# Performance work log

Hardware: AMD Instinct MI355X
Metric: run time of the kernel (lower is better)

## Reference

```python
import jax, jax.numpy as jnp
import numpy as np

NTOKEN, NINP, NHID = 50257, 256, 256
B, T = 64, 2048
RES, FC1 = 10, NHID // 3
EPS = 1e-5

def lrelu(x, p=0.01):
    return jnp.maximum(x, x * p)

def setup_inputs() -> dict:
    key = jax.random.key(0)
    ks = jax.random.split(key, 12)
    s = 0.05
    inp = {
        "input": jax.random.randint(ks[0], (B, T), 0, NTOKEN),
        "hx": jnp.zeros((B, NHID), jnp.float32),
        "cx": jnp.zeros((B, NHID), jnp.float32),
        "seq_len": jax.random.randint(ks[1], (B,), 1, T + 1),  # lengths in [1, T]
        "emb_w": jax.random.uniform(ks[2], (NTOKEN, NINP), jnp.float32, -0.1, 0.1),
        "W_ih": jax.random.normal(ks[3], (4 * NHID, NINP), jnp.float32) * s,
        "W_hh": jax.random.normal(ks[4], (4 * NHID, NHID), jnp.float32) * s,
        "b_ih": jnp.zeros((4 * NHID,), jnp.float32),
        "b_hh": jnp.zeros((4 * NHID,), jnp.float32),
        "rfc1_w": jax.random.normal(ks[5], (RES, NHID), jnp.float32) * s,
        "rfc1_b": jnp.zeros((RES,), jnp.float32),
        "rbn_g": jnp.ones((RES,), jnp.float32),
        "rbn_b": jnp.zeros((RES,), jnp.float32),
        "rbn_rm": jnp.zeros((RES,), jnp.float32),
        "rbn_rv": jnp.ones((RES,), jnp.float32),
        "rfc2_w": jax.random.normal(ks[6], (NHID, RES), jnp.float32) * s,
        "rfc2_b": jnp.zeros((NHID,), jnp.float32),
        "fc1_w": jax.random.normal(ks[7], (FC1, NHID), jnp.float32) * s,
        "fc1_b": jnp.zeros((FC1,), jnp.float32),
        "bn1_g": jnp.ones((FC1,), jnp.float32),
        "bn1_b": jnp.zeros((FC1,), jnp.float32),
        "bn1_rm": jnp.zeros((FC1,), jnp.float32),
        "bn1_rv": jnp.ones((FC1,), jnp.float32),
        "fc2_w": jax.random.normal(ks[8], (2, FC1), jnp.float32) * s,
        "fc2_b": jnp.zeros((2,), jnp.float32),
    }
    return inp

def reference(input, hx, cx, seq_len, emb_w, W_ih, W_hh, b_ih, b_hh,
              rfc1_w, rfc1_b, rbn_g, rbn_b, rbn_rm, rbn_rv, rfc2_w, rfc2_b,
              fc1_w, fc1_b, bn1_g, bn1_b, bn1_rm, bn1_rv, fc2_w, fc2_b):
    # eval mode: dropout = identity, noise = 0, BatchNorm uses running stats
    emb = emb_w[input.T]  # [T, B, ninp]
    # precompute input-side gates once (batched matmul) -> [T, B, 4*nhid]
    x_gates = jnp.einsum('tbi,gi->tbg', emb, W_ih) + b_ih + b_hh

    def step(carry, xg):
        h, c = carry
        gates = xg + h @ W_hh.T
        i, f, g, o = jnp.split(gates, 4, axis=-1)
        c = jax.nn.sigmoid(f) * c + jax.nn.sigmoid(i) * jnp.tanh(g)
        h = jax.nn.sigmoid(o) * jnp.tanh(c)
        return (h, c), h

    (hx_f, cx_f), outs = jax.lax.scan(step, (hx, cx), x_gates)  # outs: [T, B, nhid]

    # ragged mean pooling over first seq_len[b] steps
    mask = (jnp.arange(T)[:, None] < seq_len[None, :]).astype(outs.dtype)  # [T, B]
    feature = jnp.einsum('tbh,tb->bh', outs, mask) / seq_len[:, None].astype(outs.dtype)

    # ResNet block (eval)
    res = jax.nn.relu(feature) @ rfc1_w.T + rfc1_b
    res = jax.nn.relu(res)
    res = (res - rbn_rm) * jax.lax.rsqrt(rbn_rv + EPS) * rbn_g + rbn_b
    feature = feature + res @ rfc2_w.T + rfc2_b

    # classifier head
    fc = feature @ fc1_w.T + fc1_b
    fc = (fc - bn1_rm) * jax.lax.rsqrt(bn1_rv + EPS) * bn1_g + bn1_b
    fc = lrelu(fc)
    logits = fc @ fc2_w.T + fc2_b
    logp = jax.nn.log_softmax(logits, axis=-1)
    return (logp, hx_f, cx_f)
```

## Files before the change

### kernel.cpp

```cpp
#include <hip/hip_runtime.h>
#include <cstdint>


#define NTOKEN 50257
#define NINP 256
#define NHID 256
#define BB 64
#define TT 2048
#define NRES 10
#define NFC1 85
#define EPSV 1e-5f

typedef _Float16 f16;
typedef _Float16 f16x2 __attribute__((ext_vector_type(2)));
typedef _Float16 f16x8 __attribute__((ext_vector_type(8)));
typedef float f32x4 __attribute__((ext_vector_type(4)));

static __device__ __forceinline__ float sigm(float x) { return 1.0f / (1.0f + __expf(-x)); }
static __device__ __forceinline__ float tanh_(float x) {
  float ax = fabsf(x);
  float e = __expf(-2.0f * ax);
  float t = (1.0f - e) / (1.0f + e);
  return x < 0.0f ? -t : t;
}

static __device__ __forceinline__ float fdot2(f16x2 a, f16x2 b, float c) {
#if __has_builtin(__builtin_amdgcn_fdot2)
  return __builtin_amdgcn_fdot2(a, b, c, false);
#else
  return c + (float)a[0] * (float)b[0] + (float)a[1] * (float)b[1];
#endif
}

__global__ void k0_convert(const float* __restrict__ emb_w, const float* __restrict__ W_ih,
                           const float* __restrict__ b_ih, const float* __restrict__ b_hh,
                           f16* __restrict__ emb16, f16* __restrict__ wih16,
                           float* __restrict__ bias) {
  int64_t i = (int64_t)blockIdx.x * blockDim.x + threadIdx.x;
  if (i < (int64_t)NTOKEN * NINP) emb16[i] = (f16)emb_w[i];
  if (i < 4 * NHID * NINP) wih16[i] = (f16)W_ih[i];
  if (i < 4 * NHID) bias[i] = b_ih[i] + b_hh[i];
}

__global__ __launch_bounds__(256) void k1_gemm(const f16* __restrict__ emb16,
                                               const f16* __restrict__ wih16,
                                               const float* __restrict__ bias,
                                               f16* __restrict__ xgtab) {
  __shared__ __align__(16) f16 a_lds[64][40];
  __shared__ __align__(16) f16 b_lds[256][40];
  const int mt = blockIdx.x;
  const int nt0 = blockIdx.y * 256;
  const int tid = threadIdx.x;
  const int lane = tid & 63;
  const int w = tid >> 6;
  const int quad = lane >> 4;
  const int l16 = lane & 15;

  f32x4 acc[16];
#pragma unroll
  for (int i = 0; i < 16; i++) acc[i] = (f32x4){0.f, 0.f, 0.f, 0.f};

  const int ar = tid >> 2;
  int av = mt * 64 + ar;
  if (av > NTOKEN - 1) av = NTOKEN - 1;
  const int ac = (tid & 3) * 8;

  for (int kb = 0; kb < 256; kb += 32) {
    *(uint4*)&a_lds[ar][ac] = *(const uint4*)&emb16[av * 256 + kb + ac];
    {
      const uint4* bs = (const uint4*)&wih16[(nt0 + tid) * 256 + kb];
      uint4* bd = (uint4*)&b_lds[tid][0];
      bd[0] = bs[0]; bd[1] = bs[1]; bd[2] = bs[2]; bd[3] = bs[3];
    }
    __syncthreads();
    f16x8 af = *(const f16x8*)&a_lds[w * 16 + l16][quad * 8];
#pragma unroll
    for (int nt = 0; nt < 16; nt++) {
      f16x8 bf = *(const f16x8*)&b_lds[nt * 16 + l16][quad * 8];
      acc[nt] = __builtin_amdgcn_mfma_f32_16x16x32_f16(af, bf, acc[nt], 0, 0, 0);
    }
    __syncthreads();
  }
#pragma unroll
  for (int nt = 0; nt < 16; nt++) {
#pragma unroll
    for (int rg = 0; rg < 4; rg++) {
      int v = mt * 64 + w * 16 + quad * 4 + rg;
      if (v < NTOKEN) {
        int n = nt0 + nt * 16 + l16;
        xgtab[v * 1024 + n] = (f16)(acc[nt][rg] + bias[n]);
      }
    }
  }
}

#define RK 92
#define LK 36
__global__ __launch_bounds__(512, 2) void k2_rnn(
    const int* __restrict__ input, const float* __restrict__ hx0,
    const float* __restrict__ cx0, const int* __restrict__ seq_len,
    const float* __restrict__ Whh, const f16* __restrict__ xgtab,
    float* __restrict__ feat, float* __restrict__ out_hx, float* __restrict__ out_cx) {
  __shared__ uint2 lw2[LK * 512];
  __shared__ __align__(8) f16 hpak[NHID];
  __shared__ float fo_f[NHID];
  __shared__ float fo_o[NHID];

  const int b = blockIdx.x;
  const int tid = threadIdx.x;
  const int lane = tid & 63;
  const int r0 = tid, r1 = tid + 512;

  unsigned int w0[RK], w1[RK];
#pragma unroll
  for (int m = 0; m < RK; m++) {
    float2 a = *(const float2*)&Whh[r0 * 256 + 2 * m];
    float2 d = *(const float2*)&Whh[r1 * 256 + 2 * m];
    f16x2 pa; pa[0] = (f16)a.x; pa[1] = (f16)a.y;
    f16x2 pd; pd[0] = (f16)d.x; pd[1] = (f16)d.y;
    w0[m] = __builtin_bit_cast(unsigned int, pa);
    w1[m] = __builtin_bit_cast(unsigned int, pd);
  }
#pragma unroll
  for (int m = RK; m < 128; m++) {
    float2 a = *(const float2*)&Whh[r0 * 256 + 2 * m];
    float2 d = *(const float2*)&Whh[r1 * 256 + 2 * m];
    f16x2 pa; pa[0] = (f16)a.x; pa[1] = (f16)a.y;
    f16x2 pd; pd[0] = (f16)d.x; pd[1] = (f16)d.y;
    lw2[(m - RK) * 512 + tid] =
        make_uint2(__builtin_bit_cast(unsigned int, pa), __builtin_bit_cast(unsigned int, pd));
  }

  float c = 0.0f, pool = 0.0f, hnew = 0.0f;
  if (tid < NHID) {
    hpak[tid] = (f16)hx0[b * NHID + tid];
    c = cx0[b * NHID + tid];
  }
  const int L = seq_len[b];
  __syncthreads();

  const unsigned int* hpu = (const unsigned int*)hpak;
  unsigned int h2a = hpu[lane];
  unsigned int h2b = hpu[64 + lane];

  const int* tokp = input + b * TT;
  int tok_next = tokp[1];
  f16 xga, xgb;
  {
    int tok0 = tokp[0];
    xga = xgtab[tok0 * 1024 + r0];
    xgb = xgtab[tok0 * 1024 + r1];
  }

  for (int t = 0; t < TT; t++) {
    int tn = (t + 2 < TT) ? tokp[t + 2] : 0;
    f16 pfa = xgtab[tok_next * 1024 + r0];
    f16 pfb = xgtab[tok_next * 1024 + r1];

    float a0l = (float)xga, a1l = (float)xgb;
    float a0h = 0.f, a1h = 0.f;

#pragma unroll
    for (int m = 0; m < 64; m++) {
      f16x2 hh = __builtin_bit_cast(f16x2,
          (unsigned int)__builtin_amdgcn_readlane((int)h2a, m));
      a0l = fdot2(__builtin_bit_cast(f16x2, w0[m]), hh, a0l);
      a1l = fdot2(__builtin_bit_cast(f16x2, w1[m]), hh, a1l);
    }
#pragma unroll
    for (int m = 64; m < RK; m++) {
      f16x2 hh = __builtin_bit_cast(f16x2,
          (unsigned int)__builtin_amdgcn_readlane((int)h2b, m - 64));
      a0h = fdot2(__builtin_bit_cast(f16x2, w0[m]), hh, a0h);
      a1h = fdot2(__builtin_bit_cast(f16x2, w1[m]), hh, a1h);
    }
#pragma unroll
    for (int m = RK; m < 128; m++) {
      f16x2 hh = __builtin_bit_cast(f16x2,
          (unsigned int)__builtin_amdgcn_readlane((int)h2b, m - 64));
      uint2 ww = lw2[(m - RK) * 512 + tid];
      a0h = fdot2(__builtin_bit_cast(f16x2, ww.x), hh, a0h);
      a1h = fdot2(__builtin_bit_cast(f16x2, ww.y), hh, a1h);
    }
    float acc0 = a0l + a0h;
    float acc1 = a1l + a1h;

    float p = 0.f;
    if (tid >= NHID) {
      fo_f[tid - NHID] = sigm(acc0);
      fo_o[tid - NHID] = sigm(acc1);
    } else {
      p = sigm(acc0) * tanh_(acc1);
    }
    __syncthreads();
    if (tid < NHID) {
      c = fo_f[tid] * c + p;
      hnew = fo_o[tid] * tanh_(c);
      pool += (t < L) ? hnew : 0.f;
      hpak[tid] = (f16)hnew;
    }
    __syncthreads();
    h2a = hpu[lane];
    h2b = hpu[64 + lane];
    xga = pfa; xgb = pfb; tok_next = tn;
  }

  if (tid < NHID) {
    feat[b * NHID + tid] = pool / (float)L;
    out_hx[b * NHID + tid] = hnew;
    out_cx[b * NHID + tid] = c;
  }
}

__global__ __launch_bounds__(256) void k3_head(const float* __restrict__ feat,
    const float* __restrict__ rfc1_w, const float* __restrict__ rfc1_b,
    const float* __restrict__ rbn_g, const float* __restrict__ rbn_b,
    const float* __restrict__ rbn_rm, const float* __restrict__ rbn_rv,
    const float* __restrict__ rfc2_w, const float* __restrict__ rfc2_b,
    const float* __restrict__ fc1_w, const float* __restrict__ fc1_b,
    const float* __restrict__ bn1_g, const float* __restrict__ bn1_b,
    const float* __restrict__ bn1_rm, const float* __restrict__ bn1_rv,
    const float* __restrict__ fc2_w, const float* __restrict__ fc2_b,
    float* __restrict__ logp) {
  __shared__ float f[256];
  __shared__ float f2[256];
  __shared__ float res[16];
  __shared__ float fcv[96];
  const int b = blockIdx.x, tid = threadIdx.x;
  const int wv = tid >> 6, lane = tid & 63;
  f[tid] = feat[b * 256 + tid];
  __syncthreads();
  for (int r = wv; r < NRES; r += 4) {
    float p = 0.f;
#pragma unroll
    for (int j0 = 0; j0 < 4; j0++) {
      int j = lane * 4 + j0;
      p += fmaxf(f[j], 0.f) * rfc1_w[r * 256 + j];
    }
    for (int off = 32; off > 0; off >>= 1) p += __shfl_down(p, off);
    if (lane == 0) {
      float x = p + rfc1_b[r];
      x = fmaxf(x, 0.f);
      x = (x - rbn_rm[r]) * rsqrtf(rbn_rv[r] + EPSV) * rbn_g[r] + rbn_b[r];
      res[r] = x;
    }
  }
  __syncthreads();
  {
    float s = rfc2_b[tid];
#pragma unroll
    for (int r = 0; r < NRES; r++) s += res[r] * rfc2_w[tid * NRES + r];
    f2[tid] = f[tid] + s;
  }
  __syncthreads();
  for (int o = wv; o < NFC1; o += 4) {
    float p = 0.f;
#pragma unroll
    for (int j0 = 0; j0 < 4; j0++) {
      int j = lane * 4 + j0;
      p += f2[j] * fc1_w[o * 256 + j];
    }
    for (int off = 32; off > 0; off >>= 1) p += __shfl_down(p, off);
    if (lane == 0) {
      float x = p + fc1_b[o];
      x = (x - bn1_rm[o]) * rsqrtf(bn1_rv[o] + EPSV) * bn1_g[o] + bn1_b[o];
      x = fmaxf(x, 0.01f * x);
      fcv[o] = x;
    }
  }
  __syncthreads();
  if (tid == 0) {
    float l0 = fc2_b[0], l1 = fc2_b[1];
    for (int o2 = 0; o2 < NFC1; o2++) {
      l0 += fcv[o2] * fc2_w[o2];
      l1 += fcv[o2] * fc2_w[NFC1 + o2];
    }
    float mx = fmaxf(l0, l1);
    float lse = mx + __logf(__expf(l0 - mx) + __expf(l1 - mx));
    logp[b * 2 + 0] = l0 - lse;
    logp[b * 2 + 1] = l1 - lse;
  }
}

extern "C" void kernel_launch(void* const* d_in, const int* in_sizes, int n_in,
                              void* d_out, int out_size, void* d_ws, size_t ws_size,
                              hipStream_t stream) {
  const int*   input  = (const int*)  d_in[0];
  const float* hx     = (const float*)d_in[1];
  const float* cx     = (const float*)d_in[2];
  const int*   seqlen = (const int*)  d_in[3];
  const float* emb_w  = (const float*)d_in[4];
  const float* W_ih   = (const float*)d_in[5];
  const float* W_hh   = (const float*)d_in[6];
  const float* b_ih   = (const float*)d_in[7];
  const float* b_hh   = (const float*)d_in[8];
  const float* rfc1_w = (const float*)d_in[9];
  const float* rfc1_b = (const float*)d_in[10];
  const float* rbn_g  = (const float*)d_in[11];
  const float* rbn_b  = (const float*)d_in[12];
  const float* rbn_rm = (const float*)d_in[13];
  const float* rbn_rv = (const float*)d_in[14];
  const float* rfc2_w = (const float*)d_in[15];
  const float* rfc2_b = (const float*)d_in[16];
  const float* fc1_w  = (const float*)d_in[17];
  const float* fc1_b  = (const float*)d_in[18];
  const float* bn1_g  = (const float*)d_in[19];
  const float* bn1_b  = (const float*)d_in[20];
  const float* bn1_rm = (const float*)d_in[21];
  const float* bn1_rv = (const float*)d_in[22];
  const float* fc2_w  = (const float*)d_in[23];
  const float* fc2_b  = (const float*)d_in[24];

  char* ws = (char*)d_ws;
  f16*   emb16 = (f16*)(ws);
  f16*   wih16 = (f16*)(ws + 25731584);
  float* bias  = (float*)(ws + 26255872);
  f16*   xgtab = (f16*)(ws + 26259968);
  float* feat  = (float*)(ws + 129186304);

  float* out = (float*)d_out;

  k0_convert<<<dim3(NTOKEN), 256, 0, stream>>>(emb_w, W_ih, b_ih, b_hh, emb16, wih16, bias);
  k1_gemm<<<dim3((NTOKEN + 63) / 64, 4), 256, 0, stream>>>(emb16, wih16, bias, xgtab);
  k2_rnn<<<dim3(BB), 512, 0, stream>>>(input, hx, cx, seqlen, W_hh, xgtab, feat,
                                       out + 128, out + 128 + BB * NHID);
  k3_head<<<dim3(BB), 256, 0, stream>>>(feat, rfc1_w, rfc1_b, rbn_g, rbn_b, rbn_rm, rbn_rv,
                                        rfc2_w, rfc2_b, fc1_w, fc1_b, bn1_g, bn1_b, bn1_rm,
                                        bn1_rv, fc2_w, fc2_b, out);
}
```

Baseline: 4.274 ms.

## Split W_hh across registers, LDS and streamed global loads in LSTM recurrence

```diff
diff --git a/kernel.cpp b/kernel.cpp
--- a/kernel.cpp
+++ b/kernel.cpp
@@ -24,11 +24,12 @@
   return x < 0.0f ? -t : t;
 }
 
-static __device__ __forceinline__ float fdot2(f16x2 a, f16x2 b, float c) {
+static __device__ __forceinline__ float fdot2u(unsigned int a, unsigned int b, float c) {
 #if __has_builtin(__builtin_amdgcn_fdot2)
-  return __builtin_amdgcn_fdot2(a, b, c, false);
+  return __builtin_amdgcn_fdot2(__builtin_bit_cast(f16x2, a), __builtin_bit_cast(f16x2, b), c, false);
 #else
-  return c + (float)a[0] * (float)b[0] + (float)a[1] * (float)b[1];
+  f16x2 av = __builtin_bit_cast(f16x2, a), bv = __builtin_bit_cast(f16x2, b);
+  return c + (float)av[0] * (float)bv[0] + (float)av[1] * (float)bv[1];
 #endif
 }
 
@@ -94,14 +95,36 @@
   }
 }
 
-#define RK 92
-#define LK 36
+__global__ __launch_bounds__(128) void k0b_pack(const float* __restrict__ Whh,
+                                                unsigned int* __restrict__ wreg,
+                                                unsigned int* __restrict__ wlds,
+                                                unsigned int* __restrict__ wstr) {
+  const int r = blockIdx.x;
+  const int j = threadIdx.x;
+  float2 a = *(const float2*)&Whh[r * 256 + 2 * j];
+  f16x2 p; p[0] = (f16)a.x; p[1] = (f16)a.y;
+  unsigned int u = __builtin_bit_cast(unsigned int, p);
+  if (j < 64) {
+    wreg[j * 1024 + r] = u;
+  } else if (j < 100) {
+    int q = (j - 64) >> 1;
+    wlds[(q * 512 + (r & 511)) * 4 + ((j & 1) * 2) + (r >> 9)] = u;
+  } else {
+    int g = (j - 100) >> 1;
+    wstr[(g * 1024 + r) * 2 + (j & 1)] = u;
+  }
+}
+
+#define RP 64
+#define LQ 18
+#define SG 14
 __global__ __launch_bounds__(512, 2) void k2_rnn(
     const int* __restrict__ input, const float* __restrict__ hx0,
     const float* __restrict__ cx0, const int* __restrict__ seq_len,
-    const float* __restrict__ Whh, const f16* __restrict__ xgtab,
+    const unsigned int* __restrict__ wreg, const uint4* __restrict__ wldsg,
+    const uint2* __restrict__ wstr, const f16* __restrict__ xgtab,
     float* __restrict__ feat, float* __restrict__ out_hx, float* __restrict__ out_cx) {
-  __shared__ uint2 lw2[LK * 512];
+  __shared__ uint4 lw4[LQ * 512];
   __shared__ __align__(8) f16 hpak[NHID];
   __shared__ float fo_f[NHID];
   __shared__ float fo_o[NHID];
@@ -111,25 +134,14 @@
   const int lane = tid & 63;
   const int r0 = tid, r1 = tid + 512;
 
-  unsigned int w0[RK], w1[RK];
-#pragma unroll
-  for (int m = 0; m < RK; m++) {
-    float2 a = *(const float2*)&Whh[r0 * 256 + 2 * m];
-    float2 d = *(const float2*)&Whh[r1 * 256 + 2 * m];
-    f16x2 pa; pa[0] = (f16)a.x; pa[1] = (f16)a.y;
-    f16x2 pd; pd[0] = (f16)d.x; pd[1] = (f16)d.y;
-    w0[m] = __builtin_bit_cast(unsigned int, pa);
-    w1[m] = __builtin_bit_cast(unsigned int, pd);
-  }
-#pragma unroll
-  for (int m = RK; m < 128; m++) {
-    float2 a = *(const float2*)&Whh[r0 * 256 + 2 * m];
-    float2 d = *(const float2*)&Whh[r1 * 256 + 2 * m];
-    f16x2 pa; pa[0] = (f16)a.x; pa[1] = (f16)a.y;
-    f16x2 pd; pd[0] = (f16)d.x; pd[1] = (f16)d.y;
-    lw2[(m - RK) * 512 + tid] =
-        make_uint2(__builtin_bit_cast(unsigned int, pa), __builtin_bit_cast(unsigned int, pd));
-  }
+  unsigned int w0[RP], w1[RP];
+#pragma unroll
+  for (int m = 0; m < RP; m++) {
+    w0[m] = wreg[m * 1024 + tid];
+    w1[m] = wreg[m * 1024 + 512 + tid];
+  }
+#pragma unroll
+  for (int q = 0; q < LQ; q++) lw4[q * 512 + tid] = wldsg[q * 512 + tid];
 
   float c = 0.0f, pool = 0.0f, hnew = 0.0f;
   if (tid < NHID) {
@@ -144,44 +156,91 @@
   unsigned int h2b = hpu[64 + lane];
 
   const int* tokp = input + b * TT;
-  int tok_next = tokp[1];
+  int tok_next = __builtin_amdgcn_readfirstlane(tokp[1]);
   f16 xga, xgb;
   {
-    int tok0 = tokp[0];
+    int tok0 = __builtin_amdgcn_readfirstlane(tokp[0]);
     xga = xgtab[tok0 * 1024 + r0];
     xgb = xgtab[tok0 * 1024 + r1];
   }
 
+  int toffL = 0, toffS = 0;
+#pragma unroll 1
   for (int t = 0; t < TT; t++) {
-    int tn = (t + 2 < TT) ? tokp[t + 2] : 0;
-    f16 pfa = xgtab[tok_next * 1024 + r0];
-    f16 pfb = xgtab[tok_next * 1024 + r1];
+    int tn = (t + 2 < TT) ? __builtin_amdgcn_readfirstlane(tokp[t + 2]) : 0;
+    const f16* tp = xgtab + (size_t)tok_next * 1024;
+    f16 pfa = tp[r0];
+    f16 pfb = tp[r1];
 
     float a0l = (float)xga, a1l = (float)xgb;
     float a0h = 0.f, a1h = 0.f;
 
-#pragma unroll
-    for (int m = 0; m < 64; m++) {
-      f16x2 hh = __builtin_bit_cast(f16x2,
-          (unsigned int)__builtin_amdgcn_readlane((int)h2a, m));
-      a0l = fdot2(__builtin_bit_cast(f16x2, w0[m]), hh, a0l);
-      a1l = fdot2(__builtin_bit_cast(f16x2, w1[m]), hh, a1l);
-    }
-#pragma unroll
-    for (int m = 64; m < RK; m++) {
-      f16x2 hh = __builtin_bit_cast(f16x2,
-          (unsigned int)__builtin_amdgcn_readlane((int)h2b, m - 64));
-      a0h = fdot2(__builtin_bit_cast(f16x2, w0[m]), hh, a0h);
-      a1h = fdot2(__builtin_bit_cast(f16x2, w1[m]), hh, a1h);
-    }
-#pragma unroll
-    for (int m = RK; m < 128; m++) {
-      f16x2 hh = __builtin_bit_cast(f16x2,
-          (unsigned int)__builtin_amdgcn_readlane((int)h2b, m - 64));
-      uint2 ww = lw2[(m - RK) * 512 + tid];
-      a0h = fdot2(__builtin_bit_cast(f16x2, ww.x), hh, a0h);
-      a1h = fdot2(__builtin_bit_cast(f16x2, ww.y), hh, a1h);
-    }
+    uint2 sA0[7], sA1[7]; int geA[7];
+#pragma unroll
+    for (int s = 0; s < 7; s++) {
+      int ge = s + toffS; if (ge >= SG) ge -= SG;
+      geA[s] = ge;
+      sA0[s] = wstr[ge * 1024 + tid];
+      sA1[s] = wstr[ge * 1024 + 512 + tid];
+    }
+
+#pragma unroll
+    for (int m = 0; m < 32; m++) {
+      unsigned int hs = (unsigned int)__builtin_amdgcn_readlane((int)h2a, m);
+      a0l = fdot2u(w0[m], hs, a0l);
+      a1l = fdot2u(w1[m], hs, a1l);
+    }
+
+    uint2 sB0[7], sB1[7]; int geB[7];
+#pragma unroll
+    for (int s = 0; s < 7; s++) {
+      int ge = s + 7 + toffS; if (ge >= SG) ge -= SG;
+      geB[s] = ge;
+      sB0[s] = wstr[ge * 1024 + tid];
+      sB1[s] = wstr[ge * 1024 + 512 + tid];
+    }
+
+#pragma unroll
+    for (int m = 32; m < RP; m++) {
+      unsigned int hs = (unsigned int)__builtin_amdgcn_readlane((int)h2a, m);
+      a0l = fdot2u(w0[m], hs, a0l);
+      a1l = fdot2u(w1[m], hs, a1l);
+    }
+
+#pragma unroll
+    for (int s = 0; s < 7; s++) {
+      int ge = geA[s];
+      unsigned int hs0 = (unsigned int)__builtin_amdgcn_readlane((int)h2b, 36 + 2 * ge);
+      unsigned int hs1 = (unsigned int)__builtin_amdgcn_readlane((int)h2b, 37 + 2 * ge);
+      a0l = fdot2u(sA0[s].x, hs0, a0l);
+      a1l = fdot2u(sA1[s].x, hs0, a1l);
+      a0l = fdot2u(sA0[s].y, hs1, a0l);
+      a1l = fdot2u(sA1[s].y, hs1, a1l);
+    }
+
+#pragma unroll
+    for (int q = 0; q < LQ; q++) {
+      int qe = q + toffL; if (qe >= LQ) qe -= LQ;
+      uint4 w = lw4[qe * 512 + tid];
+      unsigned int hs0 = (unsigned int)__builtin_amdgcn_readlane((int)h2b, 2 * qe);
+      unsigned int hs1 = (unsigned int)__builtin_amdgcn_readlane((int)h2b, 2 * qe + 1);
+      a0h = fdot2u(w.x, hs0, a0h);
+      a1h = fdot2u(w.y, hs0, a1h);
+      a0h = fdot2u(w.z, hs1, a0h);
+      a1h = fdot2u(w.w, hs1, a1h);
+    }
+
+#pragma unroll
+    for (int s = 0; s < 7; s++) {
+      int ge = geB[s];
+      unsigned int hs0 = (unsigned int)__builtin_amdgcn_readlane((int)h2b, 36 + 2 * ge);
+      unsigned int hs1 = (unsigned int)__builtin_amdgcn_readlane((int)h2b, 37 + 2 * ge);
+      a0h = fdot2u(sB0[s].x, hs0, a0h);
+      a1h = fdot2u(sB1[s].x, hs0, a1h);
+      a0h = fdot2u(sB0[s].y, hs1, a0h);
+      a1h = fdot2u(sB1[s].y, hs1, a1h);
+    }
+
     float acc0 = a0l + a0h;
     float acc1 = a1l + a1h;
 
@@ -203,6 +262,8 @@
     h2a = hpu[lane];
     h2b = hpu[64 + lane];
     xga = pfa; xgb = pfb; tok_next = tn;
+    toffS++; if (toffS == SG) toffS = 0;
+    toffL++; if (toffL == LQ) toffL = 0;
   }
 
   if (tid < NHID) {
@@ -318,11 +379,17 @@
   f16*   xgtab = (f16*)(ws + 26259968);
   float* feat  = (float*)(ws + 129186304);
 
+  unsigned int* wreg = (unsigned int*)(ws);
+  unsigned int* wlds = (unsigned int*)(ws + 262144);
+  unsigned int* wstr = (unsigned int*)(ws + 409600);
+
   float* out = (float*)d_out;
 
   k0_convert<<<dim3(NTOKEN), 256, 0, stream>>>(emb_w, W_ih, b_ih, b_hh, emb16, wih16, bias);
   k1_gemm<<<dim3((NTOKEN + 63) / 64, 4), 256, 0, stream>>>(emb16, wih16, bias, xgtab);
-  k2_rnn<<<dim3(BB), 512, 0, stream>>>(input, hx, cx, seqlen, W_hh, xgtab, feat,
+  k0b_pack<<<dim3(1024), 128, 0, stream>>>(W_hh, wreg, wlds, wstr);
+  k2_rnn<<<dim3(BB), 512, 0, stream>>>(input, hx, cx, seqlen, wreg, (const uint4*)wlds,
+                                       (const uint2*)wstr, xgtab, feat,
                                        out + 128, out + 128 + BB * NHID);
   k3_head<<<dim3(BB), 256, 0, stream>>>(feat, rfc1_w, rfc1_b, rbn_g, rbn_b, rbn_rm, rbn_rv,
                                         rfc2_w, rfc2_b, fc1_w, fc1_b, bn1_g, bn1_b, bn1_rm,
```

After: 6.962 ms. 62.9% more time.
